# Kernel optimization log

Measured on AMD Instinct MI355X. Metric: run time of the kernel, lower is better.

The kernel has to match this reference:

```python
import jax, jax.numpy as jnp
import numpy as np

NUM_USERS = 100000
NUM_ITEMS = 200000
N_NODES = NUM_USERS + NUM_ITEMS
LATENT_DIM = 64
N_LAYERS = 3
NNZ = 4000000


def setup_inputs() -> dict:
    key = jax.random.key(0)
    k1, k2, k3, k4, k5 = jax.random.split(key, 5)
    user_emb = 0.1 * jax.random.normal(k1, (NUM_USERS, LATENT_DIM), dtype=jnp.float32)
    item_emb = 0.1 * jax.random.normal(k2, (NUM_ITEMS, LATENT_DIM), dtype=jnp.float32)
    edge_rows = jax.random.randint(k3, (NNZ,), 0, N_NODES, dtype=jnp.int32)
    edge_cols = jax.random.randint(k4, (NNZ,), 0, N_NODES, dtype=jnp.int32)
    # normalized adjacency values (positive, small, like 1/sqrt(d_i d_j))
    edge_vals = jax.random.uniform(k5, (NNZ,), dtype=jnp.float32) * 0.1
    return {"user_emb": user_emb, "item_emb": item_emb,
            "edge_rows": edge_rows, "edge_cols": edge_cols, "edge_vals": edge_vals}


def _spmm(edge_rows, edge_cols, edge_vals, x, n):
    # sparse (COO) @ dense: gather source rows, scale, scatter-add to dest rows
    msg = edge_vals[:, None] * x[edge_cols]          # [nnz, D]
    return jax.ops.segment_sum(msg, edge_rows, num_segments=n)


def reference(user_emb, item_emb, edge_rows, edge_cols, edge_vals):
    n_users = user_emb.shape[0]
    n = n_users + item_emb.shape[0]
    all_emb = jnp.concatenate([user_emb, item_emb], axis=0)  # [N, D]
    embs = [all_emb]
    for _ in range(N_LAYERS):
        all_emb = _spmm(edge_rows, edge_cols, edge_vals, all_emb, n)
        embs.append(all_emb)
    light_out = jnp.mean(jnp.stack(embs, axis=1), axis=1)   # [N, D]
    users = light_out[:n_users]
    items = light_out[n_users:]
    return users, items
```

## Files before the change

### kernel.cpp

```cpp
#include <hip/hip_runtime.h>


#define N_USERS  100000
#define N_ITEMS  200000
#define N_NODES_ 300000
#define DIM      64
#define NNZ_     4000000
#define BSHIFT   10
#define NBUCKET  ((N_NODES_ + 1023) >> 10)
#define BCAP     14336
#define PA_CHUNK 2048
#define PA_BLOCKS ((NNZ_ + PA_CHUNK - 1) / PA_CHUNK)

typedef float        f32x4 __attribute__((ext_vector_type(4)));
typedef unsigned int u32x4 __attribute__((ext_vector_type(4)));
typedef int          i32x2 __attribute__((ext_vector_type(2)));
__device__ __forceinline__ float4 ntload_f4(const float4* p) {
    f32x4 v = __builtin_nontemporal_load((const f32x4*)p);
    return make_float4(v.x, v.y, v.z, v.w);
}
__device__ __forceinline__ uint4 ntload_u4(const uint4* p) {
    u32x4 v = __builtin_nontemporal_load((const u32x4*)p);
    return make_uint4(v.x, v.y, v.z, v.w);
}
__device__ __forceinline__ int2 ntload_i2(const int2* p) {
    i32x2 v = __builtin_nontemporal_load((const i32x2*)p);
    return make_int2(v.x, v.y);
}

__device__ __forceinline__ unsigned short f2bf(float f) {
    unsigned u = __float_as_uint(f);
    unsigned r = 0x7fffu + ((u >> 16) & 1u);
    return (unsigned short)((u + r) >> 16);
}
__device__ __forceinline__ void fma8(float* acc, float v, uint4 r) {
    acc[0] = fmaf(v, __uint_as_float(r.x << 16), acc[0]);
    acc[1] = fmaf(v, __uint_as_float(r.x & 0xffff0000u), acc[1]);
    acc[2] = fmaf(v, __uint_as_float(r.y << 16), acc[2]);
    acc[3] = fmaf(v, __uint_as_float(r.y & 0xffff0000u), acc[3]);
    acc[4] = fmaf(v, __uint_as_float(r.z << 16), acc[4]);
    acc[5] = fmaf(v, __uint_as_float(r.z & 0xffff0000u), acc[5]);
    acc[6] = fmaf(v, __uint_as_float(r.w << 16), acc[6]);
    acc[7] = fmaf(v, __uint_as_float(r.w & 0xffff0000u), acc[7]);
}
__device__ __forceinline__ uint4 pack8(const float* f) {
    unsigned a = (unsigned)f2bf(f[0]) | ((unsigned)f2bf(f[1]) << 16);
    unsigned b = (unsigned)f2bf(f[2]) | ((unsigned)f2bf(f[3]) << 16);
    unsigned c = (unsigned)f2bf(f[4]) | ((unsigned)f2bf(f[5]) << 16);
    unsigned d = (unsigned)f2bf(f[6]) | ((unsigned)f2bf(f[7]) << 16);
    return make_uint4(a, b, c, d);
}
__device__ __forceinline__ void unpack8(float* f, uint4 r) {
    f[0] = __uint_as_float(r.x << 16); f[1] = __uint_as_float(r.x & 0xffff0000u);
    f[2] = __uint_as_float(r.y << 16); f[3] = __uint_as_float(r.y & 0xffff0000u);
    f[4] = __uint_as_float(r.z << 16); f[5] = __uint_as_float(r.z & 0xffff0000u);
    f[6] = __uint_as_float(r.w << 16); f[7] = __uint_as_float(r.w & 0xffff0000u);
}

__global__ void init_bf(const float4* __restrict__ u, const float4* __restrict__ it,
                        uint4* __restrict__ Abf) {
    const int n_u = N_USERS * DIM / 8;
    const int n_t = N_NODES_ * DIM / 8;
    int i = blockIdx.x * blockDim.x + threadIdx.x;
    if (i >= n_t) return;
    float4 a, b;
    if (i < n_u) { a = u[2 * i];           b = u[2 * i + 1]; }
    else         { int j = i - n_u; a = it[2 * j]; b = it[2 * j + 1]; }
    float f[8] = {a.x, a.y, a.z, a.w, b.x, b.y, b.z, b.w};
    Abf[i] = pack8(f);
}

__global__ __launch_bounds__(256) void passA(const int* __restrict__ rows,
                                             const int* __restrict__ cols,
                                             const float* __restrict__ vals,
                                             int* __restrict__ gcursor,
                                             int2* __restrict__ binned) {
    __shared__ int  hist[NBUCKET];
    __shared__ int  base_l[NBUCKET];
    __shared__ int  gshift[NBUCKET];
    __shared__ int  sc[256];
    __shared__ int2 stage[PA_CHUNK];
    __shared__ unsigned short bIdA[PA_CHUNK];

    int tid = threadIdx.x;
    int base = blockIdx.x * PA_CHUNK;
    int cnt = NNZ_ - base; if (cnt > PA_CHUNK) cnt = PA_CHUNK;

    for (int i = tid; i < NBUCKET; i += 256) hist[i] = 0;
    __syncthreads();

    int rr[8], cc[8], vv[8];
    #pragma unroll
    for (int k = 0; k < 8; ++k) {
        int i = tid + (k << 8);
        if (i < cnt) {
            int e = base + i;
            rr[k] = rows[e];
            cc[k] = cols[e];
            vv[k] = __float_as_int(vals[e]);
            atomicAdd(&hist[rr[k] >> BSHIFT], 1);
        } else rr[k] = -1;
    }
    __syncthreads();

    int i0 = 2 * tid, i1 = 2 * tid + 1;
    int c0 = (i0 < NBUCKET) ? hist[i0] : 0;
    int c1 = (i1 < NBUCKET) ? hist[i1] : 0;
    sc[tid] = c0 + c1;
    __syncthreads();
    for (int off = 1; off < 256; off <<= 1) {
        int t = (tid >= off) ? sc[tid - off] : 0;
        __syncthreads();
        sc[tid] += t;
        __syncthreads();
    }
    int excl = (tid == 0) ? 0 : sc[tid - 1];
    if (i0 < NBUCKET) {
        base_l[i0] = excl;
        int g0 = c0 ? atomicAdd(&gcursor[i0], c0) : 0;
        gshift[i0] = i0 * BCAP + g0 - excl;
        hist[i0] = 0;
    }
    if (i1 < NBUCKET) {
        base_l[i1] = excl + c0;
        int g1 = c1 ? atomicAdd(&gcursor[i1], c1) : 0;
        gshift[i1] = i1 * BCAP + g1 - (excl + c0);
        hist[i1] = 0;
    }
    __syncthreads();

    #pragma unroll
    for (int k = 0; k < 8; ++k) {
        if (rr[k] >= 0) {
            int b = rr[k] >> BSHIFT;
            int kk = atomicAdd(&hist[b], 1);
            int pos = base_l[b] + kk;
            stage[pos] = make_int2(cc[k] | ((rr[k] & 1023) << 19), vv[k]);
            bIdA[pos] = (unsigned short)b;
        }
    }
    __syncthreads();

    #pragma unroll
    for (int k = 0; k < 8; ++k) {
        int i = tid + (k << 8);
        if (i < cnt) binned[gshift[bIdA[i]] + i] = stage[i];
    }
}

__global__ __launch_bounds__(1024) void passB(const int* __restrict__ gcursor,
                                              const int2* __restrict__ binned,
                                              int* __restrict__ row_start,
                                              int2* __restrict__ sedge) {
    __shared__ int lcnt[1024];
    __shared__ int wsum[17];
    int b = blockIdx.x;
    int t = threadIdx.x;
    int lane = t & 63;
    int wid = t >> 6;
    int base = b * BCAP;
    int cnt = gcursor[b];

    int c = (t < b) ? gcursor[t] : 0;
    #pragma unroll
    for (int off = 1; off < 64; off <<= 1) c += __shfl_xor(c, off);
    if (lane == 0) wsum[wid] = c;
    __syncthreads();
    if (t < 16) {
        int s = wsum[t];
        #pragma unroll
        for (int off = 1; off < 16; off <<= 1) s += __shfl_xor(s, off);
        if (t == 0) wsum[16] = s;
    }
    lcnt[t] = 0;
    __syncthreads();
    int csr0 = wsum[16];
    if (b == NBUCKET - 1 && t == 0) row_start[N_NODES_] = NNZ_;

    int lo[14], hv[14];
    #pragma unroll
    for (int k = 0; k < 14; ++k) {
        int i = t + (k << 10);
        if (i < cnt) {
            int2 p = ntload_i2(&binned[base + i]);
            lo[k] = p.x; hv[k] = p.y;
            atomicAdd(&lcnt[((unsigned)p.x >> 19) & 1023], 1);
        } else lo[k] = -1;
    }
    __syncthreads();

    int v = lcnt[t];
    int sv = v;
    #pragma unroll
    for (int off = 1; off < 64; off <<= 1) {
        int tmp = __shfl_up(sv, off);
        if (lane >= off) sv += tmp;
    }
    if (lane == 63) wsum[wid] = sv;
    __syncthreads();
    if (t < 16) {
        int ws = wsum[t];
        #pragma unroll
        for (int off = 1; off < 16; off <<= 1) {
            int tmp = __shfl_up(ws, off);
            if (t >= off) ws += tmp;
        }
        wsum[t] = ws;
    }
    __syncthreads();
    int wbase = (wid == 0) ? 0 : wsum[wid - 1];
    int excl = wbase + sv - v;

    int gr = (b << BSHIFT) + t;
    if (gr < N_NODES_) row_start[gr] = csr0 + excl;
    lcnt[t] = excl;
    __syncthreads();

    #pragma unroll
    for (int k = 0; k < 14; ++k) {
        if (lo[k] >= 0) {
            int rl = ((unsigned)lo[k] >> 19) & 1023;
            int pos = atomicAdd(&lcnt[rl], 1);
            sedge[csr0 + pos] = make_int2(lo[k] & 0x7ffff, hv[k]);
        }
    }
}

template<bool FUSE>
__global__ __launch_bounds__(256) void spmm_bf_t(const int* __restrict__ row_start,
                                                 const int2* __restrict__ sedge,
                                                 const uint4* __restrict__ x,
                                                 uint4* __restrict__ y,
                                                 const float4* __restrict__ u,
                                                 const float4* __restrict__ it,
                                                 const uint4* __restrict__ x1,
                                                 const uint4* __restrict__ x2,
                                                 float4* __restrict__ out) {
    int w = blockIdx.x * 32 + (threadIdx.x >> 3);
    int d = threadIdx.x & 7;
    int s = row_start[w];
    int e = row_start[w + 1];
    float acc[8] = {0.f, 0.f, 0.f, 0.f, 0.f, 0.f, 0.f, 0.f};
    int i = s;
    for (; i + 1 < e; i += 2) {
        int2 p0 = sedge[i];
        int2 p1 = sedge[i + 1];
        uint4 r0 = x[((unsigned)p0.x << 3) + d];
        uint4 r1 = x[((unsigned)p1.x << 3) + d];
        fma8(acc, __int_as_float(p0.y), r0);
        fma8(acc, __int_as_float(p1.y), r1);
    }
    if (i < e) {
        int2 p0 = sedge[i];
        uint4 r0 = x[((unsigned)p0.x << 3) + d];
        fma8(acc, __int_as_float(p0.y), r0);
    }
    if (!FUSE) {
        y[(size_t)w * 8 + d] = pack8(acc);
    } else {
        const float4* src = (w < N_USERS) ? (u + (size_t)w * 16)
                                          : (it + (size_t)(w - N_USERS) * 16);
        float4 a  = ntload_f4(&src[2 * d]);
        float4 b2 = ntload_f4(&src[2 * d + 1]);
        float f0[8] = {a.x, a.y, a.z, a.w, b2.x, b2.y, b2.z, b2.w};
        float f1[8], f2[8];
        unpack8(f1, ntload_u4(&x1[(size_t)w * 8 + d]));
        unpack8(f2, x2[(size_t)w * 8 + d]);
        float o[8];
        #pragma unroll
        for (int k = 0; k < 8; ++k) o[k] = (f0[k] + f1[k] + f2[k] + acc[k]) * 0.25f;
        out[(size_t)w * 16 + 2 * d]     = make_float4(o[0], o[1], o[2], o[3]);
        out[(size_t)w * 16 + 2 * d + 1] = make_float4(o[4], o[5], o[6], o[7]);
    }
}

extern "C" void kernel_launch(void* const* d_in, const int* in_sizes, int n_in,
                              void* d_out, int out_size, void* d_ws, size_t ws_size,
                              hipStream_t stream) {
    const float* user_emb = (const float*)d_in[0];
    const float* item_emb = (const float*)d_in[1];
    const int*   rows     = (const int*)d_in[2];
    const int*   cols     = (const int*)d_in[3];
    const float* vals     = (const float*)d_in[4];
    float* out = (float*)d_out;

    const size_t nE = (size_t)N_NODES_ * DIM;
    unsigned short* Abf = (unsigned short*)d_ws;
    unsigned short* Bbf = Abf + nE;
    unsigned short* Cbf = Bbf + nE;
    int* row_start   = (int*)(Cbf + nE);
    int* gcursor     = row_start + (N_NODES_ + 2);
    int2* binned = (int2*)(gcursor + 512);
    int2* sedge  = binned + (size_t)NBUCKET * BCAP;

    const int n_t8 = (int)(nE / 8);
    const int ew_grid   = (n_t8 + 255) / 256;
    const int spmm_grid = N_NODES_ / 32;

    hipMemsetAsync(gcursor, 0, NBUCKET * sizeof(int), stream);
    passA<<<PA_BLOCKS, 256, 0, stream>>>(rows, cols, vals, gcursor, binned);
    passB<<<NBUCKET, 1024, 0, stream>>>(gcursor, binned, row_start, sedge);

    init_bf<<<ew_grid, 256, 0, stream>>>((const float4*)user_emb, (const float4*)item_emb,
                                         (uint4*)Abf);
    spmm_bf_t<false><<<spmm_grid, 256, 0, stream>>>(row_start, sedge, (const uint4*)Abf,
                                                    (uint4*)Bbf, nullptr, nullptr,
                                                    nullptr, nullptr, nullptr);
    spmm_bf_t<false><<<spmm_grid, 256, 0, stream>>>(row_start, sedge, (const uint4*)Bbf,
                                                    (uint4*)Cbf, nullptr, nullptr,
                                                    nullptr, nullptr, nullptr);
    spmm_bf_t<true><<<spmm_grid, 256, 0, stream>>>(row_start, sedge, (const uint4*)Cbf,
                                                   nullptr,
                                                   (const float4*)user_emb,
                                                   (const float4*)item_emb,
                                                   (const uint4*)Bbf, (const uint4*)Cbf,
                                                   (float4*)out);
}
```

Baseline: 591.0 us.

## Double passA chunk and block size, use warp-shuffle scan, unroll SpMM by four

passA now runs 512 threads per block over 4096-edge chunks. Its block-wide prefix scan over the 293 buckets uses wave shuffles plus a small per-wave sum instead of a barrier-heavy LDS Hillis-Steele scan. The SpMM inner loop is unrolled to four edges per iteration so more gather loads are in flight at once. The trade-offs are more LDS per passA block, which may lower occupancy, and more registers in the SpMM kernel.

```diff
diff --git a/kernel.cpp b/kernel.cpp
--- a/kernel.cpp
+++ b/kernel.cpp
@@ -9,7 +9,7 @@
 #define BSHIFT   10
 #define NBUCKET  ((N_NODES_ + 1023) >> 10)
 #define BCAP     14336
-#define PA_CHUNK 2048
+#define PA_CHUNK 4096
 #define PA_BLOCKS ((NNZ_ + PA_CHUNK - 1) / PA_CHUNK)
 
 typedef float        f32x4 __attribute__((ext_vector_type(4)));
@@ -70,7 +70,7 @@
     Abf[i] = pack8(f);
 }
 
-__global__ __launch_bounds__(256) void passA(const int* __restrict__ rows,
+__global__ __launch_bounds__(512) void passA(const int* __restrict__ rows,
                                              const int* __restrict__ cols,
                                              const float* __restrict__ vals,
                                              int* __restrict__ gcursor,
@@ -78,21 +78,23 @@
     __shared__ int  hist[NBUCKET];
     __shared__ int  base_l[NBUCKET];
     __shared__ int  gshift[NBUCKET];
-    __shared__ int  sc[256];
+    __shared__ int  wsum[8];
     __shared__ int2 stage[PA_CHUNK];
     __shared__ unsigned short bIdA[PA_CHUNK];
 
     int tid = threadIdx.x;
+    int lane = tid & 63;
+    int wid = tid >> 6;
     int base = blockIdx.x * PA_CHUNK;
     int cnt = NNZ_ - base; if (cnt > PA_CHUNK) cnt = PA_CHUNK;
 
-    for (int i = tid; i < NBUCKET; i += 256) hist[i] = 0;
+    for (int i = tid; i < NBUCKET; i += 512) hist[i] = 0;
     __syncthreads();
 
     int rr[8], cc[8], vv[8];
     #pragma unroll
     for (int k = 0; k < 8; ++k) {
-        int i = tid + (k << 8);
+        int i = tid + (k << 9);
         if (i < cnt) {
             int e = base + i;
             rr[k] = rows[e];
@@ -103,29 +105,32 @@
     }
     __syncthreads();
 
-    int i0 = 2 * tid, i1 = 2 * tid + 1;
-    int c0 = (i0 < NBUCKET) ? hist[i0] : 0;
-    int c1 = (i1 < NBUCKET) ? hist[i1] : 0;
-    sc[tid] = c0 + c1;
-    __syncthreads();
-    for (int off = 1; off < 256; off <<= 1) {
-        int t = (tid >= off) ? sc[tid - off] : 0;
-        __syncthreads();
-        sc[tid] += t;
-        __syncthreads();
-    }
-    int excl = (tid == 0) ? 0 : sc[tid - 1];
-    if (i0 < NBUCKET) {
-        base_l[i0] = excl;
-        int g0 = c0 ? atomicAdd(&gcursor[i0], c0) : 0;
-        gshift[i0] = i0 * BCAP + g0 - excl;
-        hist[i0] = 0;
-    }
-    if (i1 < NBUCKET) {
-        base_l[i1] = excl + c0;
-        int g1 = c1 ? atomicAdd(&gcursor[i1], c1) : 0;
-        gshift[i1] = i1 * BCAP + g1 - (excl + c0);
-        hist[i1] = 0;
+    int cb = (tid < NBUCKET) ? hist[tid] : 0;
+    int sv = cb;
+    #pragma unroll
+    for (int off = 1; off < 64; off <<= 1) {
+        int tmp = __shfl_up(sv, off);
+        if (lane >= off) sv += tmp;
+    }
+    if (lane == 63) wsum[wid] = sv;
+    __syncthreads();
+    if (tid < 8) {
+        int ws = wsum[tid];
+        #pragma unroll
+        for (int off = 1; off < 8; off <<= 1) {
+            int tmp = __shfl_up(ws, off);
+            if (tid >= off) ws += tmp;
+        }
+        wsum[tid] = ws;
+    }
+    __syncthreads();
+    int wbase = wid ? wsum[wid - 1] : 0;
+    int excl = wbase + sv - cb;
+    if (tid < NBUCKET) {
+        base_l[tid] = excl;
+        int g = cb ? atomicAdd(&gcursor[tid], cb) : 0;
+        gshift[tid] = tid * BCAP + g - excl;
+        hist[tid] = 0;
     }
     __syncthreads();
 
@@ -143,7 +148,7 @@
 
     #pragma unroll
     for (int k = 0; k < 8; ++k) {
-        int i = tid + (k << 8);
+        int i = tid + (k << 9);
         if (i < cnt) binned[gshift[bIdA[i]] + i] = stage[i];
     }
 }
@@ -242,13 +247,28 @@
     int e = row_start[w + 1];
     float acc[8] = {0.f, 0.f, 0.f, 0.f, 0.f, 0.f, 0.f, 0.f};
     int i = s;
-    for (; i + 1 < e; i += 2) {
+    for (; i + 3 < e; i += 4) {
+        int2 p0 = sedge[i];
+        int2 p1 = sedge[i + 1];
+        int2 p2 = sedge[i + 2];
+        int2 p3 = sedge[i + 3];
+        uint4 r0 = x[((unsigned)p0.x << 3) + d];
+        uint4 r1 = x[((unsigned)p1.x << 3) + d];
+        uint4 r2 = x[((unsigned)p2.x << 3) + d];
+        uint4 r3 = x[((unsigned)p3.x << 3) + d];
+        fma8(acc, __int_as_float(p0.y), r0);
+        fma8(acc, __int_as_float(p1.y), r1);
+        fma8(acc, __int_as_float(p2.y), r2);
+        fma8(acc, __int_as_float(p3.y), r3);
+    }
+    if (i + 1 < e) {
         int2 p0 = sedge[i];
         int2 p1 = sedge[i + 1];
         uint4 r0 = x[((unsigned)p0.x << 3) + d];
         uint4 r1 = x[((unsigned)p1.x << 3) + d];
         fma8(acc, __int_as_float(p0.y), r0);
         fma8(acc, __int_as_float(p1.y), r1);
+        i += 2;
     }
     if (i < e) {
         int2 p0 = sedge[i];
@@ -298,7 +318,7 @@
     const int spmm_grid = N_NODES_ / 32;
 
     hipMemsetAsync(gcursor, 0, NBUCKET * sizeof(int), stream);
-    passA<<<PA_BLOCKS, 256, 0, stream>>>(rows, cols, vals, gcursor, binned);
+    passA<<<PA_BLOCKS, 512, 0, stream>>>(rows, cols, vals, gcursor, binned);
     passB<<<NBUCKET, 1024, 0, stream>>>(gcursor, binned, row_start, sedge);
 
     init_bf<<<ew_grid, 256, 0, stream>>>((const float4*)user_emb, (const float4*)item_emb,
```

New measurement: 514.4 us. 12.9% less time.
